# Optimization experiments

Hardware: AMD Instinct MI355X
Metric: run time of the kernel (lower is better)

Reference implementation:

```python
import jax, jax.numpy as jnp
import numpy as np

NEG_INF = -1e6

def setup_inputs() -> dict:
    key = jax.random.key(0)
    ks = jax.random.split(key, 7)
    B, Q, K, D, H = 16, 64, 1024, 256, 128
    return {
        "queries": jax.random.normal(ks[0], (B, Q, D), dtype=jnp.float32),
        "keys": jax.random.normal(ks[1], (B, K, D), dtype=jnp.float32),
        "values": jax.random.normal(ks[2], (B, K, D), dtype=jnp.float32),
        "valid_lens": jax.random.randint(ks[3], (B,), 1, K + 1, dtype=jnp.int32),
        "W_q": jax.random.normal(ks[4], (D, H), dtype=jnp.float32) * (1.0 / np.sqrt(D)),
        "W_k": jax.random.normal(ks[5], (D, H), dtype=jnp.float32) * (1.0 / np.sqrt(D)),
        "w_v": jax.random.normal(ks[6], (H,), dtype=jnp.float32) * (1.0 / np.sqrt(H)),
    }

def reference(queries, keys, values, valid_lens, W_q, W_k, w_v):
    # project: [B,Q,H], [B,K,H]
    q = jnp.einsum('bqd,dh->bqh', queries, W_q)
    k = jnp.einsum('bkd,dh->bkh', keys, W_k)
    # broadcast add -> tanh -> score: [B,Q,K]
    features = jnp.tanh(q[:, :, None, :] + k[:, None, :, :])  # [B,Q,K,H]
    scores = jnp.einsum('bqkh,h->bqk', features, w_v)
    # masked softmax over key axis (valid_lens per batch)
    K_len = keys.shape[1]
    mask = jnp.arange(K_len)[None, None, :] < valid_lens[:, None, None]  # [B,1,K]
    scores = jnp.where(mask, scores, NEG_INF)
    attn = jax.nn.softmax(scores, axis=-1)
    # weighted sum of values: [B,Q,Dv]  (dropout p=0 -> identity)
    return jnp.einsum('bqk,bkd->bqd', attn, values)
```

## Files before the change

### kernel.cpp

```cpp
#include <hip/hip_runtime.h>

#define DDIM 256
#define HDIM 128
#define KLEN 1024
#define SCL 2.8853900817779268f

__global__ __launch_bounds__(256) void proj_kernel(
    const float* __restrict__ queries, const float* __restrict__ keys,
    const float* __restrict__ W_q, const float* __restrict__ W_k,
    float* __restrict__ Eq, float* __restrict__ Ek)
{
    __shared__ union {
        float w[64][64];
        float t[64][33];
    } sm;

    int tid = threadIdx.x;
    int hg = tid & 31;
    int rg = tid >> 5;
    int blk = blockIdx.x;

    const float* in; const float* W; int row0, hbase, b = 0, kc0 = 0; bool iskey;
    if (blk < 1024) {
        iskey = true;
        int xcd = blk & 7, s = blk >> 3;
        b = ((s >> 6) << 3) | xcd;
        int r6 = s & 63;
        kc0   = (r6 >> 1) * 32;
        hbase = (r6 & 1) << 6;
        row0  = b * KLEN + kc0;
        in = keys; W = W_k;
    } else {
        iskey = false;
        int qrb = blk - 1024;
        row0  = (qrb >> 1) * 32;
        hbase = (qrb & 1) << 6;
        in = queries; W = W_q;
    }

    float2 acc[4];
    #pragma unroll
    for (int j = 0; j < 4; j++) acc[j] = make_float2(0.f, 0.f);

    for (int dt = 0; dt < DDIM; dt += 64) {
        __syncthreads();
        #pragma unroll
        for (int i = 0; i < 4; i++) {
            int idx = tid + 256 * i;
            int dd = idx >> 4, hl = (idx & 15) << 2;
            *(float4*)(&sm.w[dd][hl]) =
                *(const float4*)(W + (size_t)(dt + dd) * HDIM + hbase + hl);
        }
        __syncthreads();

        #pragma unroll 4
        for (int d4 = 0; d4 < 64; d4 += 4) {
            float2 wr[4];
            #pragma unroll
            for (int dd = 0; dd < 4; dd++)
                wr[dd] = *(const float2*)(&sm.w[d4 + dd][hg << 1]);
            #pragma unroll
            for (int j = 0; j < 4; j++) {
                float4 a = *(const float4*)(in + (size_t)(row0 + rg * 4 + j) * DDIM + dt + d4);
                acc[j].x = fmaf(a.x, wr[0].x, acc[j].x); acc[j].y = fmaf(a.x, wr[0].y, acc[j].y);
                acc[j].x = fmaf(a.y, wr[1].x, acc[j].x); acc[j].y = fmaf(a.y, wr[1].y, acc[j].y);
                acc[j].x = fmaf(a.z, wr[2].x, acc[j].x); acc[j].y = fmaf(a.z, wr[2].y, acc[j].y);
                acc[j].x = fmaf(a.w, wr[3].x, acc[j].x); acc[j].y = fmaf(a.w, wr[3].y, acc[j].y);
            }
        }
    }

    if (!iskey) {
        #pragma unroll
        for (int j = 0; j < 4; j++) {
            float2 o = make_float2(__builtin_amdgcn_exp2f(SCL * acc[j].x),
                                   __builtin_amdgcn_exp2f(SCL * acc[j].y));
            *(float2*)(Eq + (size_t)(row0 + rg * 4 + j) * HDIM + hbase + (hg << 1)) = o;
        }
    } else {
        __syncthreads();
        #pragma unroll
        for (int j = 0; j < 4; j++) {
            sm.t[(hg << 1) + 0][rg * 4 + j] = __builtin_amdgcn_exp2f(SCL * acc[j].x);
            sm.t[(hg << 1) + 1][rg * 4 + j] = __builtin_amdgcn_exp2f(SCL * acc[j].y);
        }
        __syncthreads();
        float* dst = Ek + (size_t)b * HDIM * KLEN + (size_t)hbase * KLEN + kc0;
        #pragma unroll
        for (int i = 0; i < 2; i++) {
            int idx = tid + 256 * i;
            int hh = idx >> 3, c = (idx & 7) << 2;
            float4 o = make_float4(sm.t[hh][c], sm.t[hh][c + 1],
                                   sm.t[hh][c + 2], sm.t[hh][c + 3]);
            *(float4*)(dst + (size_t)hh * KLEN + c) = o;
        }
    }
}

__global__ __launch_bounds__(512) void score_kernel(
    const float* __restrict__ Eq, const float* __restrict__ Ek,
    const float* __restrict__ w_v, const int* __restrict__ valid_lens,
    float* __restrict__ p)
{
    __shared__ float4 eqw[HDIM];
    __shared__ float red0[8], red1[8];

    int tid = threadIdx.x, lane = tid & 63, wav = tid >> 6;
    int blk = blockIdx.x;
    int xcd = blk & 7, s = blk >> 3;
    int b = ((s >= 32) ? 8 : 0) + xcd;
    int qp = s & 31;
    int bq0 = b * 64 + qp * 2;
    int vlen = valid_lens[b];

    if (tid < HDIM) {
        float w2 = -2.0f * w_v[tid];
        eqw[tid] = make_float4(Eq[(size_t)bq0 * HDIM + tid],
                               Eq[(size_t)(bq0 + 1) * HDIM + tid], w2, 0.f);
    }
    __syncthreads();

    int k0 = tid << 1;
    float s00 = -1e30f, s01 = -1e30f, s10 = -1e30f, s11 = -1e30f;
    if (k0 < vlen) {
        const float* ekp = Ek + (size_t)b * HDIM * KLEN + k0;
        float a00 = 0.f, a01 = 0.f, a10 = 0.f, a11 = 0.f;
        #pragma unroll 4
        for (int h = 0; h < HDIM; h++) {
            float2 ek = *(const float2*)(ekp + (size_t)h * KLEN);
            float4 e  = eqw[h];
            a00 = fmaf(e.z, __builtin_amdgcn_rcpf(fmaf(e.x, ek.x, 1.f)), a00);
            a01 = fmaf(e.z, __builtin_amdgcn_rcpf(fmaf(e.x, ek.y, 1.f)), a01);
            a10 = fmaf(e.z, __builtin_amdgcn_rcpf(fmaf(e.y, ek.x, 1.f)), a10);
            a11 = fmaf(e.z, __builtin_amdgcn_rcpf(fmaf(e.y, ek.y, 1.f)), a11);
        }
        s00 = a00; s10 = a10;
        if (k0 + 1 < vlen) { s01 = a01; s11 = a11; }
    }

    float m0 = fmaxf(s00, s01), m1 = fmaxf(s10, s11);
    #pragma unroll
    for (int off = 32; off > 0; off >>= 1) {
        m0 = fmaxf(m0, __shfl_xor(m0, off, 64));
        m1 = fmaxf(m1, __shfl_xor(m1, off, 64));
    }
    if (lane == 0) { red0[wav] = m0; red1[wav] = m1; }
    __syncthreads();
    m0 = red0[0]; m1 = red1[0];
    #pragma unroll
    for (int i = 1; i < 8; i++) {
        m0 = fmaxf(m0, red0[i]);
        m1 = fmaxf(m1, red1[i]);
    }

    float e00 = __expf(s00 - m0), e01 = __expf(s01 - m0);
    float e10 = __expf(s10 - m1), e11 = __expf(s11 - m1);
    float t0 = e00 + e01, t1 = e10 + e11;
    #pragma unroll
    for (int off = 32; off > 0; off >>= 1) {
        t0 += __shfl_xor(t0, off, 64);
        t1 += __shfl_xor(t1, off, 64);
    }
    __syncthreads();
    if (lane == 0) { red0[wav] = t0; red1[wav] = t1; }
    __syncthreads();
    t0 = red0[0]; t1 = red1[0];
    #pragma unroll
    for (int i = 1; i < 8; i++) { t0 += red0[i]; t1 += red1[i]; }
    float inv0 = 1.0f / t0, inv1 = 1.0f / t1;

    float* p0 = p + (size_t)bq0 * KLEN + k0;
    *(float2*)(p0)        = make_float2(e00 * inv0, e01 * inv0);
    *(float2*)(p0 + KLEN) = make_float2(e10 * inv1, e11 * inv1);
}

__global__ __launch_bounds__(256) void av_kernel(
    const float* __restrict__ p, const float* __restrict__ values,
    const int* __restrict__ valid_lens, float* __restrict__ part)
{
    __shared__ float pt[128][10];

    int blk = blockIdx.x;
    int xcd = blk & 7, s = blk >> 3;
    int b = ((s >> 6) << 3) | xcd;
    int r = s & 63, qt = r >> 3, kq = r & 7;
    int tid = threadIdx.x, lane = tid & 63, w = tid >> 6;
    int vlen = valid_lens[b];
    int kbeg = kq << 7;
    int kc = vlen - kbeg; kc = kc < 0 ? 0 : (kc > 128 ? 128 : kc);
    int kc4 = (kc + 3) & ~3;
    int bq0 = b * 64 + qt * 8;

    {
        int q = tid >> 5, k4 = (tid & 31) << 2;
        float4 pv = *(const float4*)(p + (size_t)(bq0 + q) * KLEN + kbeg + k4);
        pt[k4 + 0][q] = pv.x;
        pt[k4 + 1][q] = pv.y;
        pt[k4 + 2][q] = pv.z;
        pt[k4 + 3][q] = pv.w;
    }
    __syncthreads();

    const float* vb = values + ((size_t)b * KLEN + kbeg) * DDIM + (lane << 2);
    float4 a0 = make_float4(0.f, 0.f, 0.f, 0.f);
    float4 a1 = make_float4(0.f, 0.f, 0.f, 0.f);

    for (int k = 0; k < kc4; k += 4) {
        #pragma unroll
        for (int i = 0; i < 4; i++) {
            float2 pp = *(const float2*)(&pt[k + i][w << 1]);
            float4 v  = *(const float4*)(vb + (size_t)(k + i) * DDIM);
            a0.x = fmaf(pp.x, v.x, a0.x); a0.y = fmaf(pp.x, v.y, a0.y);
            a0.z = fmaf(pp.x, v.z, a0.z); a0.w = fmaf(pp.x, v.w, a0.w);
            a1.x = fmaf(pp.y, v.x, a1.x); a1.y = fmaf(pp.y, v.y, a1.y);
            a1.z = fmaf(pp.y, v.z, a1.z); a1.w = fmaf(pp.y, v.w, a1.w);
        }
    }
    float* d0 = part + ((size_t)kq * 1024 + bq0 + (w << 1)) * DDIM + (lane << 2);
    *(float4*)(d0)        = a0;
    *(float4*)(d0 + DDIM) = a1;
}

__global__ __launch_bounds__(256) void combine_kernel(
    const float* __restrict__ part, float* __restrict__ out)
{
    int i = blockIdx.x * 256 + threadIdx.x;
    const float4* p4 = (const float4*)part;
    float4 a = p4[i];
    #pragma unroll
    for (int j = 1; j < 8; j++) {
        float4 v = p4[(size_t)j * 65536 + i];
        a.x += v.x; a.y += v.y; a.z += v.z; a.w += v.w;
    }
    ((float4*)out)[i] = a;
}

extern "C" void kernel_launch(void* const* d_in, const int* in_sizes, int n_in,
                              void* d_out, int out_size, void* d_ws, size_t ws_size,
                              hipStream_t stream) {
    const float* queries    = (const float*)d_in[0];
    const float* keys       = (const float*)d_in[1];
    const float* values     = (const float*)d_in[2];
    const int*   valid_lens = (const int*)d_in[3];
    const float* W_q        = (const float*)d_in[4];
    const float* W_k        = (const float*)d_in[5];
    const float* w_v        = (const float*)d_in[6];

    float* Eq   = (float*)d_ws;
    float* Ek   = Eq + 131072;
    float* p    = Ek + 2097152;
    float* part = Ek;

    proj_kernel<<<1088, 256, 0, stream>>>(queries, keys, W_q, W_k, Eq, Ek);
    score_kernel<<<512, 512, 0, stream>>>(Eq, Ek, w_v, valid_lens, p);
    av_kernel<<<1024, 256, 0, stream>>>(p, values, valid_lens, part);
    combine_kernel<<<256, 256, 0, stream>>>(part, (float*)d_out);
}
```

Measured before the change: 166.5 us.

## Restructure projection GEMM: stage input tile in swizzled LDS, read weights as wave-uniform scalars

The projection kernel now puts a 64-row by 64-column input tile in shared memory with an XOR swizzle. The next tile is prefetched into registers while the current one is computed. The weights are read straight from global memory at wave-uniform addresses, so they can become scalar loads. Each thread computes 8 hidden outputs for one row instead of 4 rows by 2 columns, and blocks cover 64 rows by 32 hidden units. The aim is to remove the repeated uncoalesced global reads of input rows and the LDS traffic for weights. The cost is more scalar loads and a different block decomposition.

```diff
diff --git a/kernel.cpp b/kernel.cpp
--- a/kernel.cpp
+++ b/kernel.cpp
@@ -11,88 +11,105 @@
     float* __restrict__ Eq, float* __restrict__ Ek)
 {
     __shared__ union {
-        float w[64][64];
-        float t[64][33];
+        float a[64 * 64];
+        float t[32][68];
     } sm;
 
-    int tid = threadIdx.x;
-    int hg = tid & 31;
-    int rg = tid >> 5;
+    const int tid  = threadIdx.x;
+    const int lane = tid & 63;
+    const int wav  = tid >> 6;
+
     int blk = blockIdx.x;
-
-    const float* in; const float* W; int row0, hbase, b = 0, kc0 = 0; bool iskey;
+    bool iskey; int b = 0, kc0 = 0, hb, row0;
+    const float* in; const float* W;
     if (blk < 1024) {
         iskey = true;
         int xcd = blk & 7, s = blk >> 3;
         b = ((s >> 6) << 3) | xcd;
         int r6 = s & 63;
-        kc0   = (r6 >> 1) * 32;
-        hbase = (r6 & 1) << 6;
-        row0  = b * KLEN + kc0;
+        kc0 = (r6 >> 2) << 6;
+        hb  = (r6 & 3) << 5;
+        row0 = b * KLEN + kc0;
         in = keys; W = W_k;
     } else {
         iskey = false;
         int qrb = blk - 1024;
-        row0  = (qrb >> 1) * 32;
-        hbase = (qrb & 1) << 6;
+        row0 = (qrb >> 2) << 6;
+        hb   = (qrb & 3) << 5;
         in = queries; W = W_q;
     }
 
-    float2 acc[4];
-    #pragma unroll
-    for (int j = 0; j < 4; j++) acc[j] = make_float2(0.f, 0.f);
-
-    for (int dt = 0; dt < DDIM; dt += 64) {
+    const int hg8 = __builtin_amdgcn_readfirstlane(wav << 3);
+    const float* Wu = W + hb + hg8;
+
+    const int srow = tid >> 4;
+    const int sgd  = tid & 15;
+    const float* gsrc = in + (size_t)(row0 + srow) * DDIM + (sgd << 2);
+
+    float4 pf0 = *(const float4*)(gsrc);
+    float4 pf1 = *(const float4*)(gsrc + 16 * DDIM);
+    float4 pf2 = *(const float4*)(gsrc + 32 * DDIM);
+    float4 pf3 = *(const float4*)(gsrc + 48 * DDIM);
+
+    float acc[8];
+    #pragma unroll
+    for (int c = 0; c < 8; c++) acc[c] = 0.f;
+
+    const int w0 = (srow)      * 64 + ((sgd ^ ((srow)      & 7)) << 2);
+    const int w1 = (srow + 16) * 64 + ((sgd ^ ((srow + 16) & 7)) << 2);
+    const int w2 = (srow + 32) * 64 + ((sgd ^ ((srow + 32) & 7)) << 2);
+    const int w3 = (srow + 48) * 64 + ((sgd ^ ((srow + 48) & 7)) << 2);
+
+    for (int dt0 = 0; dt0 < DDIM; dt0 += 64) {
+        *(float4*)(sm.a + w0) = pf0;
+        *(float4*)(sm.a + w1) = pf1;
+        *(float4*)(sm.a + w2) = pf2;
+        *(float4*)(sm.a + w3) = pf3;
         __syncthreads();
-        #pragma unroll
-        for (int i = 0; i < 4; i++) {
-            int idx = tid + 256 * i;
-            int dd = idx >> 4, hl = (idx & 15) << 2;
-            *(float4*)(&sm.w[dd][hl]) =
-                *(const float4*)(W + (size_t)(dt + dd) * HDIM + hbase + hl);
+        if (dt0 < DDIM - 64) {
+            const float* g2 = gsrc + dt0 + 64;
+            pf0 = *(const float4*)(g2);
+            pf1 = *(const float4*)(g2 + 16 * DDIM);
+            pf2 = *(const float4*)(g2 + 32 * DDIM);
+            pf3 = *(const float4*)(g2 + 48 * DDIM);
+        }
+        const float* arow = sm.a + lane * 64;
+        const int lx = lane & 7;
+        #pragma unroll
+        for (int d4 = 0; d4 < 64; d4 += 4) {
+            float4 a = *(const float4*)(arow + ((((d4 >> 2)) ^ lx) << 2));
+            const float* wr = Wu + (size_t)(dt0 + d4) * HDIM;
+            #pragma unroll
+            for (int c = 0; c < 8; c++) acc[c] = fmaf(a.x, wr[c],            acc[c]);
+            #pragma unroll
+            for (int c = 0; c < 8; c++) acc[c] = fmaf(a.y, wr[HDIM + c],     acc[c]);
+            #pragma unroll
+            for (int c = 0; c < 8; c++) acc[c] = fmaf(a.z, wr[2 * HDIM + c], acc[c]);
+            #pragma unroll
+            for (int c = 0; c < 8; c++) acc[c] = fmaf(a.w, wr[3 * HDIM + c], acc[c]);
         }
         __syncthreads();
-
-        #pragma unroll 4
-        for (int d4 = 0; d4 < 64; d4 += 4) {
-            float2 wr[4];
-            #pragma unroll
-            for (int dd = 0; dd < 4; dd++)
-                wr[dd] = *(const float2*)(&sm.w[d4 + dd][hg << 1]);
-            #pragma unroll
-            for (int j = 0; j < 4; j++) {
-                float4 a = *(const float4*)(in + (size_t)(row0 + rg * 4 + j) * DDIM + dt + d4);
-                acc[j].x = fmaf(a.x, wr[0].x, acc[j].x); acc[j].y = fmaf(a.x, wr[0].y, acc[j].y);
-                acc[j].x = fmaf(a.y, wr[1].x, acc[j].x); acc[j].y = fmaf(a.y, wr[1].y, acc[j].y);
-                acc[j].x = fmaf(a.z, wr[2].x, acc[j].x); acc[j].y = fmaf(a.z, wr[2].y, acc[j].y);
-                acc[j].x = fmaf(a.w, wr[3].x, acc[j].x); acc[j].y = fmaf(a.w, wr[3].y, acc[j].y);
-            }
-        }
-    }
+    }
+
+    float e[8];
+    #pragma unroll
+    for (int c = 0; c < 8; c++) e[c] = __builtin_amdgcn_exp2f(SCL * acc[c]);
 
     if (!iskey) {
-        #pragma unroll
-        for (int j = 0; j < 4; j++) {
-            float2 o = make_float2(__builtin_amdgcn_exp2f(SCL * acc[j].x),
-                                   __builtin_amdgcn_exp2f(SCL * acc[j].y));
-            *(float2*)(Eq + (size_t)(row0 + rg * 4 + j) * HDIM + hbase + (hg << 1)) = o;
-        }
+        float* dst = Eq + (size_t)(row0 + lane) * HDIM + hb + hg8;
+        *(float4*)(dst)     = make_float4(e[0], e[1], e[2], e[3]);
+        *(float4*)(dst + 4) = make_float4(e[4], e[5], e[6], e[7]);
     } else {
+        #pragma unroll
+        for (int c = 0; c < 8; c++) sm.t[(wav << 3) + c][lane] = e[c];
         __syncthreads();
-        #pragma unroll
-        for (int j = 0; j < 4; j++) {
-            sm.t[(hg << 1) + 0][rg * 4 + j] = __builtin_amdgcn_exp2f(SCL * acc[j].x);
-            sm.t[(hg << 1) + 1][rg * 4 + j] = __builtin_amdgcn_exp2f(SCL * acc[j].y);
-        }
-        __syncthreads();
-        float* dst = Ek + (size_t)b * HDIM * KLEN + (size_t)hbase * KLEN + kc0;
+        float* dstb = Ek + (size_t)b * HDIM * KLEN + (size_t)hb * KLEN + kc0;
         #pragma unroll
         for (int i = 0; i < 2; i++) {
-            int idx = tid + 256 * i;
-            int hh = idx >> 3, c = (idx & 7) << 2;
-            float4 o = make_float4(sm.t[hh][c], sm.t[hh][c + 1],
-                                   sm.t[hh][c + 2], sm.t[hh][c + 3]);
-            *(float4*)(dst + (size_t)hh * KLEN + c) = o;
+            int g = tid + (i << 8);
+            int h = g >> 4, k4 = (g & 15) << 2;
+            float4 o = *(const float4*)(&sm.t[h][k4]);
+            *(float4*)(dstb + (size_t)h * KLEN + k4) = o;
         }
     }
 }
```

New measurement: 147.5 us. 11.4% less time.

## Register-tile projection GEMM with shared-memory A/W and restructure AV reduction

Applied to the files above, without the earlier changes.

The projection kernel now stages both input rows (transposed) and weights in shared memory with register prefetch of the next tile. Each thread computes a 4x4 output tile instead of reading activations straight from global memory, and blocks cover 64 rows, which halves the grid. The AV kernel splits the 128-key chunk across waves, so each wave handles 32 keys for all 8 queries, and the waves are summed through shared memory. It also drops the valid-length early exit, so it always processes all 128 keys. That adds work for masked keys, but it raises value reuse and removes the loop bound that varied from block to block.

```diff
diff --git a/kernel.cpp b/kernel.cpp
--- a/kernel.cpp
+++ b/kernel.cpp
@@ -11,88 +11,115 @@
     float* __restrict__ Eq, float* __restrict__ Ek)
 {
     __shared__ union {
-        float w[64][64];
-        float t[64][33];
+        struct { float At[64][68]; float Wt[64][64]; } s;
+        float t[64][68];
     } sm;
 
-    int tid = threadIdx.x;
-    int hg = tid & 31;
-    int rg = tid >> 5;
+    const int tid = threadIdx.x;
+    const int rg  = tid & 15;
+    const int hg  = tid >> 4;
+    const int sd  = tid & 15;
+    const int sr  = tid >> 4;
+
     int blk = blockIdx.x;
-
-    const float* in; const float* W; int row0, hbase, b = 0, kc0 = 0; bool iskey;
-    if (blk < 1024) {
+    bool iskey; int b = 0, kc0 = 0, hb, row0;
+    const float* in; const float* W;
+    if (blk < 512) {
         iskey = true;
         int xcd = blk & 7, s = blk >> 3;
-        b = ((s >> 6) << 3) | xcd;
-        int r6 = s & 63;
-        kc0   = (r6 >> 1) * 32;
-        hbase = (r6 & 1) << 6;
-        row0  = b * KLEN + kc0;
+        b = ((s >> 5) << 3) | xcd;
+        int r5 = s & 31;
+        kc0 = (r5 >> 1) << 6;
+        hb  = (r5 & 1) << 6;
+        row0 = b * KLEN + kc0;
         in = keys; W = W_k;
     } else {
         iskey = false;
-        int qrb = blk - 1024;
-        row0  = (qrb >> 1) * 32;
-        hbase = (qrb & 1) << 6;
+        int qb = blk - 512;
+        row0 = (qb >> 1) << 6;
+        hb   = (qb & 1) << 6;
         in = queries; W = W_q;
     }
 
-    float2 acc[4];
-    #pragma unroll
-    for (int j = 0; j < 4; j++) acc[j] = make_float2(0.f, 0.f);
+    const float* ga = in + (size_t)(row0 + sr) * DDIM + (sd << 2);
+    const float* gw = W + (size_t)sr * HDIM + hb + (sd << 2);
+
+    float4 pfa[4], pfw[4];
+    #pragma unroll
+    for (int i = 0; i < 4; i++) {
+        pfa[i] = *(const float4*)(ga + (size_t)(16 * i) * DDIM);
+        pfw[i] = *(const float4*)(gw + (size_t)(16 * i) * HDIM);
+    }
+
+    float acc[4][4];
+    #pragma unroll
+    for (int i = 0; i < 4; i++)
+        #pragma unroll
+        for (int j = 0; j < 4; j++) acc[i][j] = 0.f;
 
     for (int dt = 0; dt < DDIM; dt += 64) {
         __syncthreads();
         #pragma unroll
         for (int i = 0; i < 4; i++) {
-            int idx = tid + 256 * i;
-            int dd = idx >> 4, hl = (idx & 15) << 2;
-            *(float4*)(&sm.w[dd][hl]) =
-                *(const float4*)(W + (size_t)(dt + dd) * HDIM + hbase + hl);
+            sm.s.At[(sd << 2) + 0][sr + 16 * i] = pfa[i].x;
+            sm.s.At[(sd << 2) + 1][sr + 16 * i] = pfa[i].y;
+            sm.s.At[(sd << 2) + 2][sr + 16 * i] = pfa[i].z;
+            sm.s.At[(sd << 2) + 3][sr + 16 * i] = pfa[i].w;
+            *(float4*)(&sm.s.Wt[sr + 16 * i][sd << 2]) = pfw[i];
         }
         __syncthreads();
-
-        #pragma unroll 4
-        for (int d4 = 0; d4 < 64; d4 += 4) {
-            float2 wr[4];
+        if (dt < DDIM - 64) {
+            const float* ga2 = ga + dt + 64;
+            const float* gw2 = gw + (size_t)(dt + 64) * HDIM;
             #pragma unroll
-            for (int dd = 0; dd < 4; dd++)
-                wr[dd] = *(const float2*)(&sm.w[d4 + dd][hg << 1]);
+            for (int i = 0; i < 4; i++) {
+                pfa[i] = *(const float4*)(ga2 + (size_t)(16 * i) * DDIM);
+                pfw[i] = *(const float4*)(gw2 + (size_t)(16 * i) * HDIM);
+            }
+        }
+        const float* arp = &sm.s.At[0][rg << 2];
+        const float* wrp = &sm.s.Wt[0][hg << 2];
+        #pragma unroll 8
+        for (int d = 0; d < 64; d++) {
+            float4 a4 = *(const float4*)(arp + d * 68);
+            float4 w4 = *(const float4*)(wrp + d * 64);
+            float av_[4] = {a4.x, a4.y, a4.z, a4.w};
+            float wv_[4] = {w4.x, w4.y, w4.z, w4.w};
             #pragma unroll
-            for (int j = 0; j < 4; j++) {
-                float4 a = *(const float4*)(in + (size_t)(row0 + rg * 4 + j) * DDIM + dt + d4);
-                acc[j].x = fmaf(a.x, wr[0].x, acc[j].x); acc[j].y = fmaf(a.x, wr[0].y, acc[j].y);
-                acc[j].x = fmaf(a.y, wr[1].x, acc[j].x); acc[j].y = fmaf(a.y, wr[1].y, acc[j].y);
-                acc[j].x = fmaf(a.z, wr[2].x, acc[j].x); acc[j].y = fmaf(a.z, wr[2].y, acc[j].y);
-                acc[j].x = fmaf(a.w, wr[3].x, acc[j].x); acc[j].y = fmaf(a.w, wr[3].y, acc[j].y);
-            }
-        }
-    }
+            for (int i = 0; i < 4; i++)
+                #pragma unroll
+                for (int j = 0; j < 4; j++)
+                    acc[i][j] = fmaf(av_[i], wv_[j], acc[i][j]);
+        }
+    }
+
+    float e[4][4];
+    #pragma unroll
+    for (int i = 0; i < 4; i++)
+        #pragma unroll
+        for (int j = 0; j < 4; j++)
+            e[i][j] = __builtin_amdgcn_exp2f(SCL * acc[i][j]);
 
     if (!iskey) {
         #pragma unroll
-        for (int j = 0; j < 4; j++) {
-            float2 o = make_float2(__builtin_amdgcn_exp2f(SCL * acc[j].x),
-                                   __builtin_amdgcn_exp2f(SCL * acc[j].y));
-            *(float2*)(Eq + (size_t)(row0 + rg * 4 + j) * HDIM + hbase + (hg << 1)) = o;
+        for (int i = 0; i < 4; i++) {
+            float* dst = Eq + (size_t)(row0 + (rg << 2) + i) * HDIM + hb + (hg << 2);
+            *(float4*)dst = make_float4(e[i][0], e[i][1], e[i][2], e[i][3]);
         }
     } else {
         __syncthreads();
         #pragma unroll
-        for (int j = 0; j < 4; j++) {
-            sm.t[(hg << 1) + 0][rg * 4 + j] = __builtin_amdgcn_exp2f(SCL * acc[j].x);
-            sm.t[(hg << 1) + 1][rg * 4 + j] = __builtin_amdgcn_exp2f(SCL * acc[j].y);
-        }
+        for (int i = 0; i < 4; i++)
+            #pragma unroll
+            for (int j = 0; j < 4; j++)
+                sm.t[(hg << 2) + j][(rg << 2) + i] = e[i][j];
         __syncthreads();
-        float* dst = Ek + (size_t)b * HDIM * KLEN + (size_t)hbase * KLEN + kc0;
-        #pragma unroll
-        for (int i = 0; i < 2; i++) {
-            int idx = tid + 256 * i;
-            int hh = idx >> 3, c = (idx & 7) << 2;
-            float4 o = make_float4(sm.t[hh][c], sm.t[hh][c + 1],
-                                   sm.t[hh][c + 2], sm.t[hh][c + 3]);
-            *(float4*)(dst + (size_t)hh * KLEN + c) = o;
+        float* dstb = Ek + (size_t)b * HDIM * KLEN + (size_t)hb * KLEN + kc0;
+        #pragma unroll
+        for (int i = 0; i < 4; i++) {
+            int h = sr + 16 * i, k4 = sd << 2;
+            float4 o = *(const float4*)(&sm.t[h][k4]);
+            *(float4*)(dstb + (size_t)h * KLEN + k4) = o;
         }
     }
 }
@@ -176,19 +203,17 @@
 
 __global__ __launch_bounds__(256) void av_kernel(
     const float* __restrict__ p, const float* __restrict__ values,
-    const int* __restrict__ valid_lens, float* __restrict__ part)
+    float* __restrict__ part)
 {
-    __shared__ float pt[128][10];
+    __shared__ float pt[128][12];
+    __shared__ float slab[3][8][256];
 
     int blk = blockIdx.x;
     int xcd = blk & 7, s = blk >> 3;
     int b = ((s >> 6) << 3) | xcd;
     int r = s & 63, qt = r >> 3, kq = r & 7;
     int tid = threadIdx.x, lane = tid & 63, w = tid >> 6;
-    int vlen = valid_lens[b];
     int kbeg = kq << 7;
-    int kc = vlen - kbeg; kc = kc < 0 ? 0 : (kc > 128 ? 128 : kc);
-    int kc4 = (kc + 3) & ~3;
     int bq0 = b * 64 + qt * 8;
 
     {
@@ -201,24 +226,45 @@
     }
     __syncthreads();
 
-    const float* vb = values + ((size_t)b * KLEN + kbeg) * DDIM + (lane << 2);
-    float4 a0 = make_float4(0.f, 0.f, 0.f, 0.f);
-    float4 a1 = make_float4(0.f, 0.f, 0.f, 0.f);
-
-    for (int k = 0; k < kc4; k += 4) {
-        #pragma unroll
-        for (int i = 0; i < 4; i++) {
-            float2 pp = *(const float2*)(&pt[k + i][w << 1]);
-            float4 v  = *(const float4*)(vb + (size_t)(k + i) * DDIM);
-            a0.x = fmaf(pp.x, v.x, a0.x); a0.y = fmaf(pp.x, v.y, a0.y);
-            a0.z = fmaf(pp.x, v.z, a0.z); a0.w = fmaf(pp.x, v.w, a0.w);
-            a1.x = fmaf(pp.y, v.x, a1.x); a1.y = fmaf(pp.y, v.y, a1.y);
-            a1.z = fmaf(pp.y, v.z, a1.z); a1.w = fmaf(pp.y, v.w, a1.w);
-        }
-    }
-    float* d0 = part + ((size_t)kq * 1024 + bq0 + (w << 1)) * DDIM + (lane << 2);
-    *(float4*)(d0)        = a0;
-    *(float4*)(d0 + DDIM) = a1;
+    const float* vb = values + ((size_t)b * KLEN + kbeg + (w << 5)) * DDIM + (lane << 2);
+    float4 acc[8];
+    #pragma unroll
+    for (int q = 0; q < 8; q++) acc[q] = make_float4(0.f, 0.f, 0.f, 0.f);
+
+    #pragma unroll 4
+    for (int k = 0; k < 32; k++) {
+        float4 v  = *(const float4*)(vb + (size_t)k * DDIM);
+        float4 p0 = *(const float4*)(&pt[(w << 5) + k][0]);
+        float4 p1 = *(const float4*)(&pt[(w << 5) + k][4]);
+        float pq[8] = {p0.x, p0.y, p0.z, p0.w, p1.x, p1.y, p1.z, p1.w};
+        #pragma unroll
+        for (int q = 0; q < 8; q++) {
+            acc[q].x = fmaf(pq[q], v.x, acc[q].x);
+            acc[q].y = fmaf(pq[q], v.y, acc[q].y);
+            acc[q].z = fmaf(pq[q], v.z, acc[q].z);
+            acc[q].w = fmaf(pq[q], v.w, acc[q].w);
+        }
+    }
+
+    if (w > 0) {
+        #pragma unroll
+        for (int q = 0; q < 8; q++)
+            *(float4*)(&slab[w - 1][q][lane << 2]) = acc[q];
+    }
+    __syncthreads();
+    if (w == 0) {
+        #pragma unroll
+        for (int s3 = 0; s3 < 3; s3++)
+            #pragma unroll
+            for (int q = 0; q < 8; q++) {
+                float4 t = *(const float4*)(&slab[s3][q][lane << 2]);
+                acc[q].x += t.x; acc[q].y += t.y; acc[q].z += t.z; acc[q].w += t.w;
+            }
+        float* d0 = part + ((size_t)kq * 1024 + bq0) * DDIM + (lane << 2);
+        #pragma unroll
+        for (int q = 0; q < 8; q++)
+            *(float4*)(d0 + (size_t)q * DDIM) = acc[q];
+    }
 }
 
 __global__ __launch_bounds__(256) void combine_kernel(
@@ -251,8 +297,8 @@
     float* p    = Ek + 2097152;
     float* part = Ek;
 
-    proj_kernel<<<1088, 256, 0, stream>>>(queries, keys, W_q, W_k, Eq, Ek);
+    proj_kernel<<<544, 256, 0, stream>>>(queries, keys, W_q, W_k, Eq, Ek);
     score_kernel<<<512, 512, 0, stream>>>(Eq, Ek, w_v, valid_lens, p);
-    av_kernel<<<1024, 256, 0, stream>>>(p, values, valid_lens, part);
+    av_kernel<<<1024, 256, 0, stream>>>(p, values, part);
     combine_kernel<<<256, 256, 0, stream>>>(part, (float*)d_out);
 }
```

Result: faster. 148.7 us (-10.7%).

## Stage projection inputs in swizzled LDS and fuse AV split-K reduction in-block

Applied to the files above, without the earlier changes.

The projection kernel now stages both the input rows and the weight tile in shared memory with an XOR swizzle, and register-prefetches the next tile while computing the current one, using a 2x4 register tile per thread. The AV kernel is reorganised so each block covers all keys for 8 queries and a quarter of the feature dimension, splitting keys across 16 thread groups and reducing their partials in shared memory. This removes the separate combine kernel and its partial-buffer round trip. In exchange the AV kernel uses fewer blocks and more registers per thread, and pays an extra in-block reduction.

```diff
diff --git a/kernel.cpp b/kernel.cpp
--- a/kernel.cpp
+++ b/kernel.cpp
@@ -11,88 +11,124 @@
     float* __restrict__ Eq, float* __restrict__ Ek)
 {
     __shared__ union {
-        float w[64][64];
-        float t[64][33];
+        struct { float At[64 * 32]; float Wt[64 * 64]; } s;
+        float t[64][36];
     } sm;
 
-    int tid = threadIdx.x;
-    int hg = tid & 31;
-    int rg = tid >> 5;
+    const int tid = threadIdx.x;
+    const int rg  = tid & 15;
+    const int hg  = tid >> 4;
+    const int ar  = tid >> 3;
+    const int ad4 = tid & 7;
+    const int wr  = tid >> 4;
+    const int wc  = tid & 15;
+
     int blk = blockIdx.x;
-
-    const float* in; const float* W; int row0, hbase, b = 0, kc0 = 0; bool iskey;
+    bool iskey; int b = 0, kc0 = 0, hh, row0;
+    const float* in; const float* W;
     if (blk < 1024) {
         iskey = true;
         int xcd = blk & 7, s = blk >> 3;
         b = ((s >> 6) << 3) | xcd;
         int r6 = s & 63;
-        kc0   = (r6 >> 1) * 32;
-        hbase = (r6 & 1) << 6;
-        row0  = b * KLEN + kc0;
+        kc0 = (r6 >> 1) << 5;
+        hh  = (r6 & 1) << 6;
+        row0 = b * KLEN + kc0;
         in = keys; W = W_k;
     } else {
         iskey = false;
-        int qrb = blk - 1024;
-        row0  = (qrb >> 1) * 32;
-        hbase = (qrb & 1) << 6;
+        int qb = blk - 1024;
+        row0 = (qb >> 1) << 5;
+        hh   = (qb & 1) << 6;
         in = queries; W = W_q;
     }
 
-    float2 acc[4];
-    #pragma unroll
-    for (int j = 0; j < 4; j++) acc[j] = make_float2(0.f, 0.f);
+    const float* ga = in + (size_t)(row0 + ar) * DDIM + (ad4 << 2);
+    const float* gw = W + (size_t)wr * HDIM + hh + (wc << 2);
+
+    float4 pfa0 = *(const float4*)(ga);
+    float4 pfa1 = *(const float4*)(ga + 32);
+    float4 pfw[4];
+    #pragma unroll
+    for (int i = 0; i < 4; i++)
+        pfw[i] = *(const float4*)(gw + (size_t)(16 * i) * HDIM);
+
+    float acc[2][4];
+    #pragma unroll
+    for (int r = 0; r < 2; r++)
+        #pragma unroll
+        for (int j = 0; j < 4; j++) acc[r][j] = 0.f;
+
+    const int wg = ((((ar >> 2) ^ ad4) << 2) | (ar & 3));
 
     for (int dt = 0; dt < DDIM; dt += 64) {
         __syncthreads();
-        #pragma unroll
-        for (int i = 0; i < 4; i++) {
-            int idx = tid + 256 * i;
-            int dd = idx >> 4, hl = (idx & 15) << 2;
-            *(float4*)(&sm.w[dd][hl]) =
-                *(const float4*)(W + (size_t)(dt + dd) * HDIM + hbase + hl);
-        }
-        __syncthreads();
-
-        #pragma unroll 4
-        for (int d4 = 0; d4 < 64; d4 += 4) {
-            float2 wr[4];
+        sm.s.At[(4 * ad4 + 0) * 32 + wg] = pfa0.x;
+        sm.s.At[(4 * ad4 + 1) * 32 + wg] = pfa0.y;
+        sm.s.At[(4 * ad4 + 2) * 32 + wg] = pfa0.z;
+        sm.s.At[(4 * ad4 + 3) * 32 + wg] = pfa0.w;
+        sm.s.At[(4 * ad4 + 32) * 32 + wg] = pfa1.x;
+        sm.s.At[(4 * ad4 + 33) * 32 + wg] = pfa1.y;
+        sm.s.At[(4 * ad4 + 34) * 32 + wg] = pfa1.z;
+        sm.s.At[(4 * ad4 + 35) * 32 + wg] = pfa1.w;
+        #pragma unroll
+        for (int i = 0; i < 4; i++)
+            *(float4*)(&sm.s.Wt[(wr + 16 * i) * 64 + (wc << 2)]) = pfw[i];
+        __syncthreads();
+        if (dt < DDIM - 64) {
+            pfa0 = *(const float4*)(ga + dt + 64);
+            pfa1 = *(const float4*)(ga + dt + 96);
             #pragma unroll
-            for (int dd = 0; dd < 4; dd++)
-                wr[dd] = *(const float2*)(&sm.w[d4 + dd][hg << 1]);
+            for (int i = 0; i < 4; i++)
+                pfw[i] = *(const float4*)(gw + (size_t)(dt + 64 + 16 * i) * HDIM);
+        }
+        #pragma unroll
+        for (int d4 = 0; d4 < 16; d4++) {
+            const int abase = ((((rg >> 1) ^ (d4 & 7)) << 2) | ((rg & 1) << 1));
             #pragma unroll
-            for (int j = 0; j < 4; j++) {
-                float4 a = *(const float4*)(in + (size_t)(row0 + rg * 4 + j) * DDIM + dt + d4);
-                acc[j].x = fmaf(a.x, wr[0].x, acc[j].x); acc[j].y = fmaf(a.x, wr[0].y, acc[j].y);
-                acc[j].x = fmaf(a.y, wr[1].x, acc[j].x); acc[j].y = fmaf(a.y, wr[1].y, acc[j].y);
-                acc[j].x = fmaf(a.z, wr[2].x, acc[j].x); acc[j].y = fmaf(a.z, wr[2].y, acc[j].y);
-                acc[j].x = fmaf(a.w, wr[3].x, acc[j].x); acc[j].y = fmaf(a.w, wr[3].y, acc[j].y);
+            for (int dd = 0; dd < 4; dd++) {
+                float2 a2 = *(const float2*)(&sm.s.At[(4 * d4 + dd) * 32 + abase]);
+                float4 w4 = *(const float4*)(&sm.s.Wt[(4 * d4 + dd) * 64 + (hg << 2)]);
+                acc[0][0] = fmaf(a2.x, w4.x, acc[0][0]);
+                acc[0][1] = fmaf(a2.x, w4.y, acc[0][1]);
+                acc[0][2] = fmaf(a2.x, w4.z, acc[0][2]);
+                acc[0][3] = fmaf(a2.x, w4.w, acc[0][3]);
+                acc[1][0] = fmaf(a2.y, w4.x, acc[1][0]);
+                acc[1][1] = fmaf(a2.y, w4.y, acc[1][1]);
+                acc[1][2] = fmaf(a2.y, w4.z, acc[1][2]);
+                acc[1][3] = fmaf(a2.y, w4.w, acc[1][3]);
             }
         }
     }
 
+    float e[2][4];
+    #pragma unroll
+    for (int r = 0; r < 2; r++)
+        #pragma unroll
+        for (int j = 0; j < 4; j++)
+            e[r][j] = __builtin_amdgcn_exp2f(SCL * acc[r][j]);
+
     if (!iskey) {
         #pragma unroll
-        for (int j = 0; j < 4; j++) {
-            float2 o = make_float2(__builtin_amdgcn_exp2f(SCL * acc[j].x),
-                                   __builtin_amdgcn_exp2f(SCL * acc[j].y));
-            *(float2*)(Eq + (size_t)(row0 + rg * 4 + j) * HDIM + hbase + (hg << 1)) = o;
+        for (int r = 0; r < 2; r++) {
+            float* dst = Eq + (size_t)(row0 + 2 * rg + r) * HDIM + hh + (hg << 2);
+            *(float4*)dst = make_float4(e[r][0], e[r][1], e[r][2], e[r][3]);
         }
     } else {
         __syncthreads();
         #pragma unroll
-        for (int j = 0; j < 4; j++) {
-            sm.t[(hg << 1) + 0][rg * 4 + j] = __builtin_amdgcn_exp2f(SCL * acc[j].x);
-            sm.t[(hg << 1) + 1][rg * 4 + j] = __builtin_amdgcn_exp2f(SCL * acc[j].y);
-        }
-        __syncthreads();
-        float* dst = Ek + (size_t)b * HDIM * KLEN + (size_t)hbase * KLEN + kc0;
+        for (int r = 0; r < 2; r++)
+            #pragma unroll
+            for (int j = 0; j < 4; j++)
+                sm.t[(hg << 2) + j][(rg << 1) + r] = e[r][j];
+        __syncthreads();
+        float* dstb = Ek + (size_t)b * HDIM * KLEN + (size_t)hh * KLEN + kc0;
         #pragma unroll
         for (int i = 0; i < 2; i++) {
-            int idx = tid + 256 * i;
-            int hh = idx >> 3, c = (idx & 7) << 2;
-            float4 o = make_float4(sm.t[hh][c], sm.t[hh][c + 1],
-                                   sm.t[hh][c + 2], sm.t[hh][c + 3]);
-            *(float4*)(dst + (size_t)hh * KLEN + c) = o;
+            int slot = tid + (i << 8);
+            int h = slot >> 3, gk = slot & 7;
+            float4 o = *(const float4*)(&sm.t[h][gk << 2]);
+            *(float4*)(dstb + (size_t)h * KLEN + (gk << 2)) = o;
         }
     }
 }
@@ -176,63 +212,72 @@
 
 __global__ __launch_bounds__(256) void av_kernel(
     const float* __restrict__ p, const float* __restrict__ values,
-    const int* __restrict__ valid_lens, float* __restrict__ part)
+    const int* __restrict__ valid_lens, float* __restrict__ out)
 {
-    __shared__ float pt[128][10];
+    __shared__ union {
+        float  pt[8][260];
+        float4 slab[16][8][16];
+    } sm;
 
     int blk = blockIdx.x;
     int xcd = blk & 7, s = blk >> 3;
-    int b = ((s >> 6) << 3) | xcd;
-    int r = s & 63, qt = r >> 3, kq = r & 7;
-    int tid = threadIdx.x, lane = tid & 63, w = tid >> 6;
+    int b = ((s >> 5) << 3) | xcd;
+    int r = s & 31, qt = r >> 2, dh = r & 3;
+    int tid = threadIdx.x;
+    int kgroup = tid >> 4, dslot = tid & 15;
     int vlen = valid_lens[b];
-    int kbeg = kq << 7;
-    int kc = vlen - kbeg; kc = kc < 0 ? 0 : (kc > 128 ? 128 : kc);
-    int kc4 = (kc + 3) & ~3;
     int bq0 = b * 64 + qt * 8;
 
-    {
-        int q = tid >> 5, k4 = (tid & 31) << 2;
-        float4 pv = *(const float4*)(p + (size_t)(bq0 + q) * KLEN + kbeg + k4);
-        pt[k4 + 0][q] = pv.x;
-        pt[k4 + 1][q] = pv.y;
-        pt[k4 + 2][q] = pv.z;
-        pt[k4 + 3][q] = pv.w;
-    }
-    __syncthreads();
-
-    const float* vb = values + ((size_t)b * KLEN + kbeg) * DDIM + (lane << 2);
-    float4 a0 = make_float4(0.f, 0.f, 0.f, 0.f);
-    float4 a1 = make_float4(0.f, 0.f, 0.f, 0.f);
-
-    for (int k = 0; k < kc4; k += 4) {
-        #pragma unroll
-        for (int i = 0; i < 4; i++) {
-            float2 pp = *(const float2*)(&pt[k + i][w << 1]);
-            float4 v  = *(const float4*)(vb + (size_t)(k + i) * DDIM);
-            a0.x = fmaf(pp.x, v.x, a0.x); a0.y = fmaf(pp.x, v.y, a0.y);
-            a0.z = fmaf(pp.x, v.z, a0.z); a0.w = fmaf(pp.x, v.w, a0.w);
-            a1.x = fmaf(pp.y, v.x, a1.x); a1.y = fmaf(pp.y, v.y, a1.y);
-            a1.z = fmaf(pp.y, v.z, a1.z); a1.w = fmaf(pp.y, v.w, a1.w);
-        }
-    }
-    float* d0 = part + ((size_t)kq * 1024 + bq0 + (w << 1)) * DDIM + (lane << 2);
-    *(float4*)(d0)        = a0;
-    *(float4*)(d0 + DDIM) = a1;
-}
-
-__global__ __launch_bounds__(256) void combine_kernel(
-    const float* __restrict__ part, float* __restrict__ out)
-{
-    int i = blockIdx.x * 256 + threadIdx.x;
-    const float4* p4 = (const float4*)part;
-    float4 a = p4[i];
-    #pragma unroll
-    for (int j = 1; j < 8; j++) {
-        float4 v = p4[(size_t)j * 65536 + i];
-        a.x += v.x; a.y += v.y; a.z += v.z; a.w += v.w;
-    }
-    ((float4*)out)[i] = a;
+    float4 acc4[8];
+    #pragma unroll
+    for (int q = 0; q < 8; q++) acc4[q] = make_float4(0.f, 0.f, 0.f, 0.f);
+
+    for (int c = 0; c < 4; c++) {
+        __syncthreads();
+        #pragma unroll
+        for (int i = 0; i < 2; i++) {
+            int slot = tid + (i << 8);
+            int q = slot >> 6, k4 = slot & 63;
+            float4 pv = *(const float4*)(p + (size_t)(bq0 + q) * KLEN + (c << 8) + (k4 << 2));
+            *(float4*)(&sm.pt[q][k4 << 2]) = pv;
+        }
+        __syncthreads();
+
+        int kg = (c << 8) + (kgroup << 4);
+        int cnt = vlen - kg; cnt = cnt < 0 ? 0 : (cnt > 16 ? 16 : cnt);
+        int cnt4 = (cnt + 3) & ~3;
+        const float* vp = values + ((size_t)b * KLEN + kg) * DDIM + (dh << 6) + (dslot << 2);
+        for (int j = 0; j < cnt4; j += 4) {
+            #pragma unroll
+            for (int jj = 0; jj < 4; jj++) {
+                int kl = (kgroup << 4) + j + jj;
+                float4 v = *(const float4*)(vp + (size_t)(j + jj) * DDIM);
+                #pragma unroll
+                for (int q = 0; q < 8; q++) {
+                    float pq = sm.pt[q][kl];
+                    acc4[q].x = fmaf(pq, v.x, acc4[q].x);
+                    acc4[q].y = fmaf(pq, v.y, acc4[q].y);
+                    acc4[q].z = fmaf(pq, v.z, acc4[q].z);
+                    acc4[q].w = fmaf(pq, v.w, acc4[q].w);
+                }
+            }
+        }
+    }
+
+    __syncthreads();
+    #pragma unroll
+    for (int q = 0; q < 8; q++) sm.slab[kgroup][q][dslot] = acc4[q];
+    __syncthreads();
+    if (tid < 128) {
+        int q = tid >> 4, ds = tid & 15;
+        float4 a = sm.slab[0][q][ds];
+        #pragma unroll
+        for (int g = 1; g < 16; g++) {
+            float4 t = sm.slab[g][q][ds];
+            a.x += t.x; a.y += t.y; a.z += t.z; a.w += t.w;
+        }
+        *(float4*)(out + (size_t)(bq0 + q) * DDIM + (dh << 6) + (ds << 2)) = a;
+    }
 }
 
 extern "C" void kernel_launch(void* const* d_in, const int* in_sizes, int n_in,
@@ -249,10 +294,8 @@
     float* Eq   = (float*)d_ws;
     float* Ek   = Eq + 131072;
     float* p    = Ek + 2097152;
-    float* part = Ek;
 
     proj_kernel<<<1088, 256, 0, stream>>>(queries, keys, W_q, W_k, Eq, Ek);
     score_kernel<<<512, 512, 0, stream>>>(Eq, Ek, w_v, valid_lens, p);
-    av_kernel<<<1024, 256, 0, stream>>>(p, values, valid_lens, part);
-    combine_kernel<<<256, 256, 0, stream>>>(part, (float*)d_out);
+    av_kernel<<<512, 256, 0, stream>>>(p, values, valid_lens, (float*)d_out);
 }
```

Result: no change. 168.9 us (+1.5%).
